# Optimization experiments

Hardware: AMD Instinct MI355X
Metric: run time of the kernel (lower is better)

Reference implementation:

```python
import jax, jax.numpy as jnp
import numpy as np

N = 100000
E = 1600000
IN_DIM = 4
HIDDEN = 64
OUT = 32
HEADS = 4
NEG_SLOPE = 0.2


def setup_inputs() -> dict:
    key = jax.random.key(0)
    ks = jax.random.split(key, 12)
    C1 = HIDDEN // HEADS  # 16 per-head channels in conv1
    inp = {
        "x": jax.random.normal(ks[0], (N, IN_DIM), dtype=jnp.float32),
        "edge_index": jax.random.randint(ks[1], (2, E), 0, N, dtype=jnp.int64),
        # conv1 (GATv2, heads=4, out_channels=16, concat)
        "Wl1": jax.random.normal(ks[2], (IN_DIM, HEADS * C1), dtype=jnp.float32) * 0.3,
        "Wr1": jax.random.normal(ks[3], (IN_DIM, HEADS * C1), dtype=jnp.float32) * 0.3,
        "att1": jax.random.normal(ks[4], (HEADS, C1), dtype=jnp.float32) * 0.3,
        "b1": jax.random.normal(ks[5], (HEADS * C1,), dtype=jnp.float32) * 0.1,
        "g1": jnp.ones((HIDDEN,), dtype=jnp.float32),
        "be1": jnp.zeros((HIDDEN,), dtype=jnp.float32),
        # conv2 (GATv2, heads=1, out_channels=32)
        "Wl2": jax.random.normal(ks[6], (HIDDEN, OUT), dtype=jnp.float32) * 0.1,
        "Wr2": jax.random.normal(ks[7], (HIDDEN, OUT), dtype=jnp.float32) * 0.1,
        "att2": jax.random.normal(ks[8], (1, OUT), dtype=jnp.float32) * 0.3,
        "b2": jax.random.normal(ks[9], (OUT,), dtype=jnp.float32) * 0.1,
        "g2": jnp.ones((OUT,), dtype=jnp.float32),
        "be2": jnp.zeros((OUT,), dtype=jnp.float32),
    }
    return inp


def gatv2_conv(x, Wl, Wr, att, bias, src, dst, heads, out_ch):
    # x: [N, F_in]; lin_l for source messages, lin_r for target (PyG GATv2Conv defaults)
    xl = (x @ Wl).reshape(N, heads, out_ch)  # [N,H,C]
    xr = (x @ Wr).reshape(N, heads, out_ch)
    m = xl[src] + xr[dst]                                     # [E,H,C] gather
    e = jnp.sum(jax.nn.leaky_relu(m, NEG_SLOPE) * att, axis=-1)  # [E,H]
    # segment softmax over destination node
    emax = jax.ops.segment_max(e, dst, num_segments=N)        # [N,H]
    ee = jnp.exp(e - emax[dst])
    denom = jax.ops.segment_sum(ee, dst, num_segments=N)      # [N,H]
    alpha = ee / denom[dst]
    out = jax.ops.segment_sum(xl[src] * alpha[..., None], dst, num_segments=N)  # [N,H,C]
    return out.reshape(N, heads * out_ch) + bias


def layer_norm(x, gamma, beta, eps=1e-5):
    mu = jnp.mean(x, axis=-1, keepdims=True)
    var = jnp.var(x, axis=-1, keepdims=True)
    return (x - mu) * jax.lax.rsqrt(var + eps) * gamma + beta


def reference(x, edge_index, Wl1, Wr1, att1, b1, g1, be1, Wl2, Wr2, att2, b2, g2, be2):
    src, dst = edge_index[0], edge_index[1]
    h = gatv2_conv(x, Wl1, Wr1, att1, b1, src, dst, HEADS, HIDDEN // HEADS)
    h = jax.nn.elu(layer_norm(h, g1, be1))
    h = gatv2_conv(h, Wl2, Wr2, att2, b2, src, dst, 1, OUT)
    return layer_norm(h, g2, be2)
```

## Files before the change

kernel.cpp:

```cpp
#include <hip/hip_runtime.h>
#include <math.h>

#define NN 100000
#define NE 1600000
#define HID 64
#define OUTC 32
#define NBUCK 196
#define NPB 512
#define EPB 3125
#define LOG2E 1.44269504088896340736f

typedef float f32x2 __attribute__((ext_vector_type(2)));

__device__ __forceinline__ f32x2 pk_mul(f32x2 a, f32x2 b) {
    f32x2 r;
    asm("v_pk_mul_f32 %0, %1, %2" : "=v"(r) : "v"(a), "v"(b));
    return r;
}
__device__ __forceinline__ f32x2 pk_fma(f32x2 a, f32x2 b, f32x2 c) {
    f32x2 r;
    asm("v_pk_fma_f32 %0, %1, %2, %3" : "=v"(r) : "v"(a), "v"(b), "v"(c));
    return r;
}
__device__ __forceinline__ f32x2 pk_add(f32x2 a, f32x2 b) {
    f32x2 r;
    asm("v_pk_add_f32 %0, %1, %2" : "=v"(r) : "v"(a), "v"(b));
    return r;
}
__device__ __forceinline__ f32x2 pk_fma_blo(f32x2 x, f32x2 b, f32x2 c) {
    f32x2 r;
    asm("v_pk_fma_f32 %0, %1, %2, %3 op_sel:[0,0,0] op_sel_hi:[0,1,1]" : "=v"(r) : "v"(x), "v"(b), "v"(c));
    return r;
}
__device__ __forceinline__ f32x2 pk_fma_bhi(f32x2 x, f32x2 b, f32x2 c) {
    f32x2 r;
    asm("v_pk_fma_f32 %0, %1, %2, %3 op_sel:[1,0,0] op_sel_hi:[1,1,1]" : "=v"(r) : "v"(x), "v"(b), "v"(c));
    return r;
}
__device__ __forceinline__ f32x2 pk_mul_bhi(f32x2 x, f32x2 b) {
    f32x2 r;
    asm("v_pk_mul_f32 %0, %1, %2 op_sel:[1,0] op_sel_hi:[1,1]" : "=v"(r) : "v"(x), "v"(b));
    return r;
}
__device__ __forceinline__ f32x2 pk_abs(f32x2 a) {
    f32x2 r;
    r.x = __builtin_fabsf(a.x);
    r.y = __builtin_fabsf(a.y);
    return r;
}
__device__ __forceinline__ unsigned short f2bf(float f) {
    unsigned int u = __float_as_uint(f);
    u += 0x7FFFu + ((u >> 16) & 1u);
    return (unsigned short)(u >> 16);
}
__device__ __forceinline__ float quad_add_xor1(float v) {
    int t = __builtin_amdgcn_mov_dpp(__float_as_int(v), 0xB1, 0xF, 0xF, true);
    return v + __int_as_float(t);
}
__device__ __forceinline__ float quad_add_xor2(float v) {
    int t = __builtin_amdgcn_mov_dpp(__float_as_int(v), 0x4E, 0xF, 0xF, true);
    return v + __int_as_float(t);
}
__device__ __forceinline__ float ex2(float v) {
    float r;
    asm("v_exp_f32 %0, %1" : "=v"(r) : "v"(v));
    return r;
}


__global__ __launch_bounds__(256) void bucketA_kernel(const int* __restrict__ ei,
                                                      int* __restrict__ gcount,
                                                      int* __restrict__ blkcnt) {
    __shared__ int cnt[NBUCK];
    int tid = threadIdx.x;
    for (int i = tid; i < NBUCK; i += 256) cnt[i] = 0;
    __syncthreads();
    int base = blockIdx.x * EPB;
    const int* dstp = ei + NE;
    for (int i = tid; i < EPB; i += 256) atomicAdd(&cnt[dstp[base + i] >> 9], 1);
    __syncthreads();
    for (int i = tid; i < NBUCK; i += 256) {
        blkcnt[i * NPB + blockIdx.x] = cnt[i];
        atomicAdd(&gcount[i], cnt[i]);
    }
}

__global__ __launch_bounds__(256) void scanBlk_kernel(const int* __restrict__ gcount,
                                                      const int* __restrict__ blkcnt,
                                                      int* __restrict__ cursors,
                                                      int* __restrict__ gbase_arr) {
    __shared__ int sbuf[256];
    __shared__ int swave[4];
    int b = blockIdx.x;
    int tid = threadIdx.x;
    int gv = (tid < b) ? gcount[tid] : 0;
    for (int off = 1; off < 64; off <<= 1) gv += __shfl_xor(gv, off);
    if ((tid & 63) == 0) swave[tid >> 6] = gv;
    __syncthreads();
    int gbase = swave[0] + swave[1] + swave[2] + swave[3];
    int c0 = blkcnt[b * NPB + 2 * tid];
    int c1 = blkcnt[b * NPB + 2 * tid + 1];
    int tsum = c0 + c1;
    int run = tsum;
    sbuf[tid] = tsum;
    __syncthreads();
    for (int off = 1; off < 256; off <<= 1) {
        int u = (tid >= off) ? sbuf[tid - off] : 0;
        __syncthreads();
        run += u;
        sbuf[tid] = run;
        __syncthreads();
    }
    int excl = gbase + run - tsum;
    cursors[b * NPB + 2 * tid] = excl;
    cursors[b * NPB + 2 * tid + 1] = excl + c0;
    if (tid == 0) {
        gbase_arr[b] = gbase;
        if (b == 0) gbase_arr[NBUCK] = NE;
    }
}

__global__ __launch_bounds__(256) void bucketB_kernel(const int* __restrict__ ei,
                                                      const int* __restrict__ cursors,
                                                      unsigned int* __restrict__ staging) {
    __shared__ int cur[NBUCK];
    int tid = threadIdx.x;
    for (int i = tid; i < NBUCK; i += 256) cur[i] = cursors[i * NPB + blockIdx.x];
    __syncthreads();
    int base = blockIdx.x * EPB;
    const int* dstp = ei + NE;
    for (int i = tid; i < EPB; i += 256) {
        int d = dstp[base + i];
        int s = ei[base + i];
        int pos = atomicAdd(&cur[d >> 9], 1);
        staging[pos] = ((unsigned int)(d & 511) << 17) | (unsigned int)s;
    }
}

__global__ __launch_bounds__(256) void bucketC_kernel(const unsigned int* __restrict__ staging,
                                                      const int* __restrict__ gbase,
                                                      int* __restrict__ rowptr,
                                                      int* __restrict__ csr_src) {
    int b = blockIdx.x;
    int node0 = b << 9;
    int nnode = min(512, NN - node0);
    int e0 = gbase[b], e1 = gbase[b + 1];
    __shared__ int deg[512];
    __shared__ int sbuf[256];
    int tid = threadIdx.x;
    deg[tid] = 0;
    deg[tid + 256] = 0;
    __syncthreads();
    for (int e = e0 + tid; e < e1; e += 256) atomicAdd(&deg[staging[e] >> 17], 1);
    __syncthreads();
    int d0 = deg[2 * tid], d1 = deg[2 * tid + 1];
    int tsum = d0 + d1;
    int run = tsum;
    sbuf[tid] = tsum;
    __syncthreads();
    for (int off = 1; off < 256; off <<= 1) {
        int u = (tid >= off) ? sbuf[tid - off] : 0;
        __syncthreads();
        run += u;
        sbuf[tid] = run;
        __syncthreads();
    }
    int eb = run - tsum;
    deg[2 * tid] = eb;
    deg[2 * tid + 1] = eb + d0;
    if (2 * tid < nnode) rowptr[node0 + 2 * tid] = e0 + eb;
    if (2 * tid + 1 < nnode) rowptr[node0 + 2 * tid + 1] = e0 + eb + d0;
    if (b == NBUCK - 1 && tid == 0) rowptr[NN] = NE;
    __syncthreads();
    for (int e = e0 + tid; e < e1; e += 256) {
        unsigned int p = staging[e];
        int dl = p >> 17;
        int src = (int)(p & 0x1FFFFu);
        int pos = e0 + atomicAdd(&deg[dl], 1);
        csr_src[pos] = src;
    }
}


#define PROC1(X, IDX, MASKED)                                                 \
    {                                                                         \
        f32x2 Xxy = {X.x, X.y}, Xzw = {X.z, X.w};                             \
        f32x2 s01 = pk_fma_blo(Xxy, wl0_01, pk_fma_bhi(Xxy, wl1_01,           \
                    pk_fma_blo(Xzw, wl2_01, pk_fma_bhi(Xzw, wl3_01, xr01)))); \
        f32x2 s23 = pk_fma_blo(Xxy, wl0_23, pk_fma_bhi(Xxy, wl1_23,           \
                    pk_fma_blo(Xzw, wl2_23, pk_fma_bhi(Xzw, wl3_23, xr23)))); \
        f32x2 t01 = pk_abs(s01), t23 = pk_abs(s23);                           \
        f32x2 dd = pk_fma(s01, a06_01, pk_fma(t01, a04_01,                    \
                   pk_fma(s23, a06_23, pk_mul(t23, a04_23))));                \
        float vv = dd.x + dd.y;                                               \
        vv = quad_add_xor1(vv);                                               \
        vv = quad_add_xor2(vv);   \
        float ev = ex2(vv);                                                   \
        if (MASKED && (IDX) >= cnt) ev = 0.f;                                 \
        ssum += ev;                                                           \
        f32x2 ev2 = {ev, ev};                                                 \
        accA = pk_fma(ev2, Xxy, accA);                                        \
        accB = pk_fma(ev2, Xzw, accB);                                        \
    }

__global__ __launch_bounds__(256) void gather1_kernel(const int* __restrict__ rowptr,
                                                      const int* __restrict__ csr_src,
                                                      const float* __restrict__ x,
                                                      const float* __restrict__ Wl,
                                                      const float* __restrict__ Wr,
                                                      const float* __restrict__ att,
                                                      const float* __restrict__ b1,
                                                      const float* __restrict__ g1,
                                                      const float* __restrict__ be1,
                                                      float* __restrict__ h) {
    __shared__ float sWl[4 * HID], sWr[4 * HID];
    __shared__ float satt[HID], sb[HID], sg[HID], sbe[HID];
    int tid = threadIdx.x;
    if (tid < 256) {
        sWl[tid] = Wl[tid];
        sWr[tid] = Wr[tid];
    }
    if (tid < HID) {
        satt[tid] = att[tid];
        sb[tid] = b1[tid];
        sg[tid] = g1[tid];
        sbe[tid] = be1[tid];
    }
    __syncthreads();
    int node = blockIdx.x * 8 + (tid >> 5);
    int lane = tid & 63;
    int hbase = lane & 32;
    int ln = lane & 31;
    int grp = ln >> 4;
    int ch = (ln & 15) * 4;
    int p0 = rowptr[node], p1 = rowptr[node + 1];

    f32x2 wl0_01 = {sWl[ch + 0], sWl[ch + 1]},            wl0_23 = {sWl[ch + 2], sWl[ch + 3]};
    f32x2 wl1_01 = {sWl[64 + ch + 0], sWl[64 + ch + 1]},  wl1_23 = {sWl[64 + ch + 2], sWl[64 + ch + 3]};
    f32x2 wl2_01 = {sWl[128 + ch + 0], sWl[128 + ch + 1]}, wl2_23 = {sWl[128 + ch + 2], sWl[128 + ch + 3]};
    f32x2 wl3_01 = {sWl[192 + ch + 0], sWl[192 + ch + 1]}, wl3_23 = {sWl[192 + ch + 2], sWl[192 + ch + 3]};

    float4 xd = *(const float4*)(x + node * 4);
    f32x2 Dxy = {xd.x, xd.y}, Dzw = {xd.z, xd.w};
    f32x2 wr0_01 = {sWr[ch + 0], sWr[ch + 1]},            wr0_23 = {sWr[ch + 2], sWr[ch + 3]};
    f32x2 wr1_01 = {sWr[64 + ch + 0], sWr[64 + ch + 1]},  wr1_23 = {sWr[64 + ch + 2], sWr[64 + ch + 3]};
    f32x2 wr2_01 = {sWr[128 + ch + 0], sWr[128 + ch + 1]}, wr2_23 = {sWr[128 + ch + 2], sWr[128 + ch + 3]};
    f32x2 wr3_01 = {sWr[192 + ch + 0], sWr[192 + ch + 1]}, wr3_23 = {sWr[192 + ch + 2], sWr[192 + ch + 3]};
    f32x2 xr01 = pk_fma_blo(Dxy, wr0_01, pk_fma_bhi(Dxy, wr1_01,
                 pk_fma_blo(Dzw, wr2_01, pk_mul_bhi(Dzw, wr3_01))));
    f32x2 xr23 = pk_fma_blo(Dxy, wr0_23, pk_fma_bhi(Dxy, wr1_23,
                 pk_fma_blo(Dzw, wr2_23, pk_mul_bhi(Dzw, wr3_23))));

    f32x2 a06_01 = {0.6f * LOG2E * satt[ch + 0], 0.6f * LOG2E * satt[ch + 1]};
    f32x2 a06_23 = {0.6f * LOG2E * satt[ch + 2], 0.6f * LOG2E * satt[ch + 3]};
    f32x2 a04_01 = {0.4f * LOG2E * satt[ch + 0], 0.4f * LOG2E * satt[ch + 1]};
    f32x2 a04_23 = {0.4f * LOG2E * satt[ch + 2], 0.4f * LOG2E * satt[ch + 3]};

    const float4* x4 = (const float4*)x;
    float ssum = 0.f;
    f32x2 accA = {0.f, 0.f}, accB = {0.f, 0.f};
    for (int p = p0; p < p1; p += 32) {
        int cnt = min(32, p1 - p);
        int srcs = (ln < cnt) ? csr_src[p + ln] : 0;
        int j = 0;
        for (; j + 8 <= cnt; j += 8) {
            int s0 = __shfl(srcs, hbase + j + grp);
            int s1 = __shfl(srcs, hbase + j + 2 + grp);
            int s2 = __shfl(srcs, hbase + j + 4 + grp);
            int s3 = __shfl(srcs, hbase + j + 6 + grp);
            float4 X0 = x4[s0];
            float4 X1 = x4[s1];
            float4 X2 = x4[s2];
            float4 X3 = x4[s3];
            PROC1(X0, 0, 0)
            PROC1(X1, 0, 0)
            PROC1(X2, 0, 0)
            PROC1(X3, 0, 0)
        }
        for (; j < cnt; j += 2) {
            int idx = j + grp;
            int s0 = __shfl(srcs, hbase + (idx & 31));
            float4 X0 = x4[s0];
            PROC1(X0, idx, 1)
        }
    }
    float aA0 = accA.x, aA1 = accA.y, aB0 = accB.x, aB1 = accB.y;
    ssum += __shfl_xor(ssum, 16);
    aA0 += __shfl_xor(aA0, 16); aA1 += __shfl_xor(aA1, 16);
    aB0 += __shfl_xor(aB0, 16); aB1 += __shfl_xor(aB1, 16);
    f32x2 kA = {aA0, aA1}, kB = {aB0, aB1};
    f32x2 o01 = pk_fma_blo(kA, wl0_01, pk_fma_bhi(kA, wl1_01,
                pk_fma_blo(kB, wl2_01, pk_mul_bhi(kB, wl3_01))));
    f32x2 o23 = pk_fma_blo(kA, wl0_23, pk_fma_bhi(kA, wl1_23,
                pk_fma_blo(kB, wl2_23, pk_mul_bhi(kB, wl3_23))));
    float inv_s = (p1 > p0) ? __builtin_amdgcn_rcpf(ssum) : 0.f;
    float v0 = o01.x * inv_s + sb[ch + 0];
    float v1 = o01.y * inv_s + sb[ch + 1];
    float v2 = o23.x * inv_s + sb[ch + 2];
    float v3 = o23.y * inv_s + sb[ch + 3];
    float s4 = v0 + v1 + v2 + v3;
    s4 += __shfl_xor(s4, 1); s4 += __shfl_xor(s4, 2);
    s4 += __shfl_xor(s4, 4); s4 += __shfl_xor(s4, 8);
    float mu = s4 * (1.f / 64.f);
    float d0 = v0 - mu, d1 = v1 - mu, d2 = v2 - mu, d3 = v3 - mu;
    float q4 = d0 * d0 + d1 * d1 + d2 * d2 + d3 * d3;
    q4 += __shfl_xor(q4, 1); q4 += __shfl_xor(q4, 2);
    q4 += __shfl_xor(q4, 4); q4 += __shfl_xor(q4, 8);
    float inv = __builtin_amdgcn_rsqf(q4 * (1.f / 64.f) + 1e-5f);
    float y0 = d0 * inv * sg[ch + 0] + sbe[ch + 0];
    float y1 = d1 * inv * sg[ch + 1] + sbe[ch + 1];
    float y2 = d2 * inv * sg[ch + 2] + sbe[ch + 2];
    float y3 = d3 * inv * sg[ch + 3] + sbe[ch + 3];
    y0 = y0 > 0.f ? y0 : (ex2(y0 * LOG2E) - 1.f);
    y1 = y1 > 0.f ? y1 : (ex2(y1 * LOG2E) - 1.f);
    y2 = y2 > 0.f ? y2 : (ex2(y2 * LOG2E) - 1.f);
    y3 = y3 > 0.f ? y3 : (ex2(y3 * LOG2E) - 1.f);
    if (grp == 0) {
        *(float4*)(h + (size_t)node * 64 + ch) = make_float4(y0, y1, y2, y3);
    }
}


__global__ __launch_bounds__(256) void lin2_kernel(const float* __restrict__ h,
                                                   const float* __restrict__ Wl,
                                                   const float* __restrict__ Wr,
                                                   unsigned short* __restrict__ xl2b,
                                                   float* __restrict__ xr2) {
    __shared__ float sW[2 * HID * OUTC];
    __shared__ float sh[8 * HID];
    for (int i = threadIdx.x; i < HID * OUTC; i += blockDim.x) {
        sW[i] = Wl[i];
        sW[HID * OUTC + i] = Wr[i];
    }
    int node0 = blockIdx.x * 8;
    for (int i = threadIdx.x; i < 8 * HID; i += blockDim.x) {
        int n = node0 + (i >> 6);
        sh[i] = (n < NN) ? h[n * 64 + (i & 63)] : 0.f;
    }
    __syncthreads();
    int ln = threadIdx.x >> 5;
    int col = threadIdx.x & 31;
    int node = node0 + ln;
    if (node < NN) {
        float al = 0.f, ar = 0.f;
#pragma unroll
        for (int k = 0; k < HID; k++) {
            float hv = sh[ln * 64 + k];
            al += hv * sW[k * 32 + col];
            ar += hv * sW[HID * OUTC + k * 32 + col];
        }
        xl2b[node * 32 + col] = f2bf(al);
        xr2[node * 32 + col] = ar;
    }
}

#define G2_PROC(RV, IDX, MASKED)                                              \
    {                                                                         \
        f32x2 L01, L23, L45, L67;                                             \
        L01.x = __uint_as_float(RV.x << 16); L01.y = __uint_as_float(RV.x & 0xFFFF0000u); \
        L23.x = __uint_as_float(RV.y << 16); L23.y = __uint_as_float(RV.y & 0xFFFF0000u); \
        L45.x = __uint_as_float(RV.z << 16); L45.y = __uint_as_float(RV.z & 0xFFFF0000u); \
        L67.x = __uint_as_float(RV.w << 16); L67.y = __uint_as_float(RV.w & 0xFFFF0000u); \
        f32x2 s01 = pk_add(L01, xr01), s23 = pk_add(L23, xr23);               \
        f32x2 s45 = pk_add(L45, xr45), s67 = pk_add(L67, xr67);               \
        f32x2 t01 = pk_abs(s01), t23 = pk_abs(s23);                           \
        f32x2 t45 = pk_abs(s45), t67 = pk_abs(s67);                           \
        f32x2 dd = pk_fma(s01, a06_01, pk_fma(t01, a04_01,                    \
                   pk_fma(s23, a06_23, pk_fma(t23, a04_23,                    \
                   pk_fma(s45, a06_45, pk_fma(t45, a04_45,                    \
                   pk_fma(s67, a06_67, pk_mul(t67, a04_67))))))));            \
        float vv = dd.x + dd.y;                                               \
        vv = quad_add_xor1(vv);                                               \
        vv = quad_add_xor2(vv);   \
        float ev = ex2(vv);                                                   \
        if (MASKED && (IDX) >= cnt) ev = 0.f;                                 \
        ssum += ev;                                                           \
        f32x2 ev2 = {ev, ev};                                                 \
        ac01 = pk_fma(ev2, L01, ac01); ac23 = pk_fma(ev2, L23, ac23);         \
        ac45 = pk_fma(ev2, L45, ac45); ac67 = pk_fma(ev2, L67, ac67);         \
    }

__global__ __launch_bounds__(256) void gather2_kernel(const int* __restrict__ rowptr,
                                                      const int* __restrict__ csr_src,
                                                      const unsigned short* __restrict__ xl2b,
                                                      const float* __restrict__ xr2,
                                                      const float* __restrict__ att,
                                                      const float* __restrict__ b2,
                                                      const float* __restrict__ g2,
                                                      const float* __restrict__ be2,
                                                      float* __restrict__ out) {
    __shared__ float satt[OUTC], sb[OUTC], sg[OUTC], sbe[OUTC];
    int tid = threadIdx.x;
    if (tid < OUTC) {
        satt[tid] = att[tid];
        sb[tid] = b2[tid];
        sg[tid] = g2[tid];
        sbe[tid] = be2[tid];
    }
    __syncthreads();
    int node = blockIdx.x * 8 + (tid >> 5);
    int lane = tid & 63;
    int hbase = lane & 32;
    int ln = lane & 31;
    int es = ln >> 2;
    int ch = (ln & 3) * 8;
    int p0 = rowptr[node], p1 = rowptr[node + 1];

    const float* xrp = xr2 + (size_t)node * 32 + ch;
    float4 xra = *(const float4*)xrp;
    float4 xrb = *(const float4*)(xrp + 4);
    f32x2 xr01 = {xra.x, xra.y}, xr23 = {xra.z, xra.w};
    f32x2 xr45 = {xrb.x, xrb.y}, xr67 = {xrb.z, xrb.w};
    f32x2 a06_01 = {0.6f * LOG2E * satt[ch + 0], 0.6f * LOG2E * satt[ch + 1]};
    f32x2 a06_23 = {0.6f * LOG2E * satt[ch + 2], 0.6f * LOG2E * satt[ch + 3]};
    f32x2 a06_45 = {0.6f * LOG2E * satt[ch + 4], 0.6f * LOG2E * satt[ch + 5]};
    f32x2 a06_67 = {0.6f * LOG2E * satt[ch + 6], 0.6f * LOG2E * satt[ch + 7]};
    f32x2 a04_01 = {0.4f * LOG2E * satt[ch + 0], 0.4f * LOG2E * satt[ch + 1]};
    f32x2 a04_23 = {0.4f * LOG2E * satt[ch + 2], 0.4f * LOG2E * satt[ch + 3]};
    f32x2 a04_45 = {0.4f * LOG2E * satt[ch + 4], 0.4f * LOG2E * satt[ch + 5]};
    f32x2 a04_67 = {0.4f * LOG2E * satt[ch + 6], 0.4f * LOG2E * satt[ch + 7]};

    float ssum = 0.f;
    f32x2 ac01 = {0.f, 0.f}, ac23 = {0.f, 0.f}, ac45 = {0.f, 0.f}, ac67 = {0.f, 0.f};
    for (int p = p0; p < p1; p += 32) {
        int cnt = min(32, p1 - p);
        int srcs = (ln < cnt) ? csr_src[p + ln] : 0;
        int j = 0;
        for (; j + 8 <= cnt; j += 8) {
            int sa = __shfl(srcs, hbase + j + es);
            uint4 Ra = *(const uint4*)(xl2b + (size_t)sa * 32 + ch);
            G2_PROC(Ra, 0, 0)
        }
        if (j < cnt) {
            int idx = j + es;
            int sa = __shfl(srcs, hbase + (idx & 31));
            uint4 Ra = *(const uint4*)(xl2b + (size_t)sa * 32 + ch);
            G2_PROC(Ra, idx, 1)
        }
    }
    float A0 = ac01.x, A1 = ac01.y, A2 = ac23.x, A3 = ac23.y;
    float A4 = ac45.x, A5 = ac45.y, A6 = ac67.x, A7 = ac67.y;
    for (int off = 4; off < 32; off <<= 1) {
        ssum += __shfl_xor(ssum, off);
        A0 += __shfl_xor(A0, off); A1 += __shfl_xor(A1, off);
        A2 += __shfl_xor(A2, off); A3 += __shfl_xor(A3, off);
        A4 += __shfl_xor(A4, off); A5 += __shfl_xor(A5, off);
        A6 += __shfl_xor(A6, off); A7 += __shfl_xor(A7, off);
    }
    float inv_s = (p1 > p0) ? __builtin_amdgcn_rcpf(ssum) : 0.f;
    float v0 = A0 * inv_s + sb[ch + 0], v1 = A1 * inv_s + sb[ch + 1];
    float v2 = A2 * inv_s + sb[ch + 2], v3 = A3 * inv_s + sb[ch + 3];
    float v4 = A4 * inv_s + sb[ch + 4], v5 = A5 * inv_s + sb[ch + 5];
    float v6 = A6 * inv_s + sb[ch + 6], v7 = A7 * inv_s + sb[ch + 7];
    float s8 = v0 + v1 + v2 + v3 + v4 + v5 + v6 + v7;
    s8 += __shfl_xor(s8, 1); s8 += __shfl_xor(s8, 2);
    float mu = s8 * (1.f / 32.f);
    float d0 = v0 - mu, d1 = v1 - mu, d2 = v2 - mu, d3 = v3 - mu;
    float d4 = v4 - mu, d5 = v5 - mu, d6 = v6 - mu, d7 = v7 - mu;
    float q8 = d0 * d0 + d1 * d1 + d2 * d2 + d3 * d3 + d4 * d4 + d5 * d5 + d6 * d6 + d7 * d7;
    q8 += __shfl_xor(q8, 1); q8 += __shfl_xor(q8, 2);
    float inv = __builtin_amdgcn_rsqf(q8 * (1.f / 32.f) + 1e-5f);
    if (es == 0) {
        float4 oa, ob;
        oa.x = d0 * inv * sg[ch + 0] + sbe[ch + 0];
        oa.y = d1 * inv * sg[ch + 1] + sbe[ch + 1];
        oa.z = d2 * inv * sg[ch + 2] + sbe[ch + 2];
        oa.w = d3 * inv * sg[ch + 3] + sbe[ch + 3];
        ob.x = d4 * inv * sg[ch + 4] + sbe[ch + 4];
        ob.y = d5 * inv * sg[ch + 5] + sbe[ch + 5];
        ob.z = d6 * inv * sg[ch + 6] + sbe[ch + 6];
        ob.w = d7 * inv * sg[ch + 7] + sbe[ch + 7];
        *(float4*)(out + (size_t)node * 32 + ch) = oa;
        *(float4*)(out + (size_t)node * 32 + ch + 4) = ob;
    }
}

extern "C" void kernel_launch(void* const* d_in, const int* in_sizes, int n_in,
                              void* d_out, int out_size, void* d_ws, size_t ws_size,
                              hipStream_t stream) {
    const float* x    = (const float*)d_in[0];
    const int* ei     = (const int*)d_in[1];
    const float* Wl1  = (const float*)d_in[2];
    const float* Wr1  = (const float*)d_in[3];
    const float* att1 = (const float*)d_in[4];
    const float* b1   = (const float*)d_in[5];
    const float* g1   = (const float*)d_in[6];
    const float* be1  = (const float*)d_in[7];
    const float* Wl2  = (const float*)d_in[8];
    const float* Wr2  = (const float*)d_in[9];
    const float* att2 = (const float*)d_in[10];
    const float* b2   = (const float*)d_in[11];
    const float* g2   = (const float*)d_in[12];
    const float* be2  = (const float*)d_in[13];
    float* out = (float*)d_out;

    char* W = (char*)d_ws;
    float* h = (float*)W;
    unsigned short* xl2b = (unsigned short*)(W + 25600000);
    float* xr2 = (float*)(W + 32000000);
    int* rowptr = (int*)(W + 44800000);
    int* csr_src = rowptr + NN + 1;
    unsigned int* staging = (unsigned int*)(csr_src + NE);
    int* gcount = (int*)(staging + NE);
    int* gbase = gcount + NBUCK;
    int* blkcnt = gbase + NBUCK + 1;
    int* cursors = blkcnt + NBUCK * NPB;

    const int B = 256;

    hipMemsetAsync(gcount, 0, NBUCK * sizeof(int), stream);
    bucketA_kernel<<<NPB, B, 0, stream>>>(ei, gcount, blkcnt);
    scanBlk_kernel<<<NBUCK, B, 0, stream>>>(gcount, blkcnt, cursors, gbase);
    bucketB_kernel<<<NPB, B, 0, stream>>>(ei, cursors, staging);
    bucketC_kernel<<<NBUCK, B, 0, stream>>>(staging, gbase, rowptr, csr_src);

    gather1_kernel<<<NN / 8, B, 0, stream>>>(rowptr, csr_src, x, Wl1, Wr1, att1,
                                             b1, g1, be1, h);

    lin2_kernel<<<(NN + 7) / 8, B, 0, stream>>>(h, Wl2, Wr2, xl2b, xr2);
    gather2_kernel<<<NN / 8, B, 0, stream>>>(rowptr, csr_src, xl2b, xr2, att2,
                                             b2, g2, be2, out);
}
```

Before: 187.8 us.

## Fuse bucket count/scatter passes and fold lin2 into gather1

Merges the bucket counting and scatter kernels into one pass. Each block now reserves its slots with a global atomic into a fixed-capacity per-bucket staging region (MAXB), so the per-block count matrix and the 196-block scan are no longer needed and only a tiny single-block scan remains. It also fuses the layer-2 linear projection into the layer-1 gather kernel: the normalized hidden row is kept in shared memory instead of being written to and reread from global memory. This assumes no bucket exceeds MAXB edges, and it adds shared-memory weights to gather1, which may lower occupancy.

```diff
diff --git a/kernel.cpp b/kernel.cpp
--- a/kernel.cpp
+++ b/kernel.cpp
@@ -8,6 +8,7 @@
 #define NBUCK 196
 #define NPB 512
 #define EPB 3125
+#define MAXB 10240
 #define LOG2E 1.44269504088896340736f
 
 typedef float f32x2 __attribute__((ext_vector_type(2)));
@@ -68,10 +69,11 @@
 }
 
 
-__global__ __launch_bounds__(256) void bucketA_kernel(const int* __restrict__ ei,
+__global__ __launch_bounds__(256) void bucketB_kernel(const int* __restrict__ ei,
                                                       int* __restrict__ gcount,
-                                                      int* __restrict__ blkcnt) {
+                                                      unsigned int* __restrict__ staging) {
     __shared__ int cnt[NBUCK];
+    __shared__ int cur[NBUCK];
     int tid = threadIdx.x;
     for (int i = tid; i < NBUCK; i += 256) cnt[i] = 0;
     __syncthreads();
@@ -79,30 +81,24 @@
     const int* dstp = ei + NE;
     for (int i = tid; i < EPB; i += 256) atomicAdd(&cnt[dstp[base + i] >> 9], 1);
     __syncthreads();
-    for (int i = tid; i < NBUCK; i += 256) {
-        blkcnt[i * NPB + blockIdx.x] = cnt[i];
-        atomicAdd(&gcount[i], cnt[i]);
-    }
-}
-
-__global__ __launch_bounds__(256) void scanBlk_kernel(const int* __restrict__ gcount,
-                                                      const int* __restrict__ blkcnt,
-                                                      int* __restrict__ cursors,
-                                                      int* __restrict__ gbase_arr) {
+    for (int i = tid; i < NBUCK; i += 256)
+        cur[i] = i * MAXB + atomicAdd(&gcount[i], cnt[i]);
+    __syncthreads();
+    for (int i = tid; i < EPB; i += 256) {
+        int d = dstp[base + i];
+        int s = ei[base + i];
+        int pos = atomicAdd(&cur[d >> 9], 1);
+        staging[pos] = ((unsigned int)(d & 511) << 17) | (unsigned int)s;
+    }
+}
+
+__global__ __launch_bounds__(256) void scanG_kernel(const int* __restrict__ gcount,
+                                                    int* __restrict__ gbase) {
     __shared__ int sbuf[256];
-    __shared__ int swave[4];
-    int b = blockIdx.x;
     int tid = threadIdx.x;
-    int gv = (tid < b) ? gcount[tid] : 0;
-    for (int off = 1; off < 64; off <<= 1) gv += __shfl_xor(gv, off);
-    if ((tid & 63) == 0) swave[tid >> 6] = gv;
-    __syncthreads();
-    int gbase = swave[0] + swave[1] + swave[2] + swave[3];
-    int c0 = blkcnt[b * NPB + 2 * tid];
-    int c1 = blkcnt[b * NPB + 2 * tid + 1];
-    int tsum = c0 + c1;
-    int run = tsum;
-    sbuf[tid] = tsum;
+    int v = (tid < NBUCK) ? gcount[tid] : 0;
+    int run = v;
+    sbuf[tid] = run;
     __syncthreads();
     for (int off = 1; off < 256; off <<= 1) {
         int u = (tid >= off) ? sbuf[tid - off] : 0;
@@ -111,47 +107,28 @@
         sbuf[tid] = run;
         __syncthreads();
     }
-    int excl = gbase + run - tsum;
-    cursors[b * NPB + 2 * tid] = excl;
-    cursors[b * NPB + 2 * tid + 1] = excl + c0;
-    if (tid == 0) {
-        gbase_arr[b] = gbase;
-        if (b == 0) gbase_arr[NBUCK] = NE;
-    }
-}
-
-__global__ __launch_bounds__(256) void bucketB_kernel(const int* __restrict__ ei,
-                                                      const int* __restrict__ cursors,
-                                                      unsigned int* __restrict__ staging) {
-    __shared__ int cur[NBUCK];
-    int tid = threadIdx.x;
-    for (int i = tid; i < NBUCK; i += 256) cur[i] = cursors[i * NPB + blockIdx.x];
-    __syncthreads();
-    int base = blockIdx.x * EPB;
-    const int* dstp = ei + NE;
-    for (int i = tid; i < EPB; i += 256) {
-        int d = dstp[base + i];
-        int s = ei[base + i];
-        int pos = atomicAdd(&cur[d >> 9], 1);
-        staging[pos] = ((unsigned int)(d & 511) << 17) | (unsigned int)s;
-    }
+    if (tid < NBUCK) gbase[tid] = run - v;
+    if (tid == 0) gbase[NBUCK] = NE;
 }
 
 __global__ __launch_bounds__(256) void bucketC_kernel(const unsigned int* __restrict__ staging,
+                                                      const int* __restrict__ gcount,
                                                       const int* __restrict__ gbase,
                                                       int* __restrict__ rowptr,
                                                       int* __restrict__ csr_src) {
     int b = blockIdx.x;
     int node0 = b << 9;
     int nnode = min(512, NN - node0);
-    int e0 = gbase[b], e1 = gbase[b + 1];
+    int ecnt = gcount[b];
+    int e0 = gbase[b];
+    const unsigned int* st = staging + (size_t)b * MAXB;
     __shared__ int deg[512];
     __shared__ int sbuf[256];
     int tid = threadIdx.x;
     deg[tid] = 0;
     deg[tid + 256] = 0;
     __syncthreads();
-    for (int e = e0 + tid; e < e1; e += 256) atomicAdd(&deg[staging[e] >> 17], 1);
+    for (int e = tid; e < ecnt; e += 256) atomicAdd(&deg[st[e] >> 17], 1);
     __syncthreads();
     int d0 = deg[2 * tid], d1 = deg[2 * tid + 1];
     int tsum = d0 + d1;
@@ -172,8 +149,8 @@
     if (2 * tid + 1 < nnode) rowptr[node0 + 2 * tid + 1] = e0 + eb + d0;
     if (b == NBUCK - 1 && tid == 0) rowptr[NN] = NE;
     __syncthreads();
-    for (int e = e0 + tid; e < e1; e += 256) {
-        unsigned int p = staging[e];
+    for (int e = tid; e < ecnt; e += 256) {
+        unsigned int p = st[e];
         int dl = p >> 17;
         int src = (int)(p & 0x1FFFFu);
         int pos = e0 + atomicAdd(&deg[dl], 1);
@@ -212,9 +189,14 @@
                                                       const float* __restrict__ b1,
                                                       const float* __restrict__ g1,
                                                       const float* __restrict__ be1,
-                                                      float* __restrict__ h) {
+                                                      const float* __restrict__ Wl2,
+                                                      const float* __restrict__ Wr2,
+                                                      unsigned short* __restrict__ xl2b,
+                                                      float* __restrict__ xr2) {
     __shared__ float sWl[4 * HID], sWr[4 * HID];
     __shared__ float satt[HID], sb[HID], sg[HID], sbe[HID];
+    __shared__ float sW2[2 * HID * OUTC];
+    __shared__ float sh[8 * HID];
     int tid = threadIdx.x;
     if (tid < 256) {
         sWl[tid] = Wl[tid];
@@ -226,8 +208,11 @@
         sg[tid] = g1[tid];
         sbe[tid] = be1[tid];
     }
-    __syncthreads();
-    int node = blockIdx.x * 8 + (tid >> 5);
+    for (int i = tid; i < 2 * HID * OUTC; i += 256)
+        sW2[i] = (i < HID * OUTC) ? Wl2[i] : Wr2[i - HID * OUTC];
+    __syncthreads();
+    int hw = tid >> 5;
+    int node = blockIdx.x * 8 + hw;
     int lane = tid & 63;
     int hbase = lane & 32;
     int ln = lane & 31;
@@ -316,43 +301,25 @@
     y2 = y2 > 0.f ? y2 : (ex2(y2 * LOG2E) - 1.f);
     y3 = y3 > 0.f ? y3 : (ex2(y3 * LOG2E) - 1.f);
     if (grp == 0) {
-        *(float4*)(h + (size_t)node * 64 + ch) = make_float4(y0, y1, y2, y3);
-    }
-}
-
-
-__global__ __launch_bounds__(256) void lin2_kernel(const float* __restrict__ h,
-                                                   const float* __restrict__ Wl,
-                                                   const float* __restrict__ Wr,
-                                                   unsigned short* __restrict__ xl2b,
-                                                   float* __restrict__ xr2) {
-    __shared__ float sW[2 * HID * OUTC];
-    __shared__ float sh[8 * HID];
-    for (int i = threadIdx.x; i < HID * OUTC; i += blockDim.x) {
-        sW[i] = Wl[i];
-        sW[HID * OUTC + i] = Wr[i];
-    }
-    int node0 = blockIdx.x * 8;
-    for (int i = threadIdx.x; i < 8 * HID; i += blockDim.x) {
-        int n = node0 + (i >> 6);
-        sh[i] = (n < NN) ? h[n * 64 + (i & 63)] : 0.f;
-    }
-    __syncthreads();
-    int ln = threadIdx.x >> 5;
-    int col = threadIdx.x & 31;
-    int node = node0 + ln;
-    if (node < NN) {
+        *(float4*)(sh + hw * 64 + ch) = make_float4(y0, y1, y2, y3);
+    }
+    __syncthreads();
+    {
+        int nl = tid >> 5;
+        int col = tid & 31;
         float al = 0.f, ar = 0.f;
 #pragma unroll
         for (int k = 0; k < HID; k++) {
-            float hv = sh[ln * 64 + k];
-            al += hv * sW[k * 32 + col];
-            ar += hv * sW[HID * OUTC + k * 32 + col];
+            float hv = sh[nl * 64 + k];
+            al += hv * sW2[k * 32 + col];
+            ar += hv * sW2[HID * OUTC + k * 32 + col];
         }
-        xl2b[node * 32 + col] = f2bf(al);
-        xr2[node * 32 + col] = ar;
-    }
-}
+        int ng = blockIdx.x * 8 + nl;
+        xl2b[ng * 32 + col] = f2bf(al);
+        xr2[ng * 32 + col] = ar;
+    }
+}
+
 
 #define G2_PROC(RV, IDX, MASKED)                                              \
     {                                                                         \
@@ -495,29 +462,24 @@
     float* out = (float*)d_out;
 
     char* W = (char*)d_ws;
-    float* h = (float*)W;
-    unsigned short* xl2b = (unsigned short*)(W + 25600000);
-    float* xr2 = (float*)(W + 32000000);
-    int* rowptr = (int*)(W + 44800000);
+    unsigned short* xl2b = (unsigned short*)W;
+    float* xr2 = (float*)(W + 6400000);
+    int* rowptr = (int*)(W + 19200000);
     int* csr_src = rowptr + NN + 1;
     unsigned int* staging = (unsigned int*)(csr_src + NE);
-    int* gcount = (int*)(staging + NE);
+    int* gcount = (int*)(staging + (size_t)NBUCK * MAXB);
     int* gbase = gcount + NBUCK;
-    int* blkcnt = gbase + NBUCK + 1;
-    int* cursors = blkcnt + NBUCK * NPB;
 
     const int B = 256;
 
     hipMemsetAsync(gcount, 0, NBUCK * sizeof(int), stream);
-    bucketA_kernel<<<NPB, B, 0, stream>>>(ei, gcount, blkcnt);
-    scanBlk_kernel<<<NBUCK, B, 0, stream>>>(gcount, blkcnt, cursors, gbase);
-    bucketB_kernel<<<NPB, B, 0, stream>>>(ei, cursors, staging);
-    bucketC_kernel<<<NBUCK, B, 0, stream>>>(staging, gbase, rowptr, csr_src);
+    bucketB_kernel<<<NPB, B, 0, stream>>>(ei, gcount, staging);
+    scanG_kernel<<<1, B, 0, stream>>>(gcount, gbase);
+    bucketC_kernel<<<NBUCK, B, 0, stream>>>(staging, gcount, gbase, rowptr, csr_src);
 
     gather1_kernel<<<NN / 8, B, 0, stream>>>(rowptr, csr_src, x, Wl1, Wr1, att1,
-                                             b1, g1, be1, h);
-
-    lin2_kernel<<<(NN + 7) / 8, B, 0, stream>>>(h, Wl2, Wr2, xl2b, xr2);
+                                             b1, g1, be1, Wl2, Wr2, xl2b, xr2);
+
     gather2_kernel<<<NN / 8, B, 0, stream>>>(rowptr, csr_src, xl2b, xr2, att2,
                                              b2, g2, be2, out);
 }
```

New measurement: 167.2 us. 1.12x faster.
